# Kernel tuning notes

Measured on AMD Instinct MI355X. Metric: run time of the kernel, lower is better.

The kernel has to match this reference:

```python
import jax, jax.numpy as jnp
import numpy as np

N_NODES = 100000
N_EDGES = 1600000
H = 64
EPS_SM = 1e-16
NEG_SLOPE = 0.01  # LeakyReLU default
BN_EPS = 1e-5


def leaky_relu(x):
    return jnp.where(x >= 0, x, NEG_SLOPE * x)


def transformer_conv(x, src, tgt, edge_attr, Wq, bq, Wk, bk, Wv, bv, We, Ws, bs):
    # PyG TransformerConv, heads=1, concat=True, root_weight=True, lin_edge bias=False
    n = x.shape[0]
    q = x @ Wq + bq            # [N,H]
    k = x @ Wk + bk            # [N,H]
    v = x @ Wv + bv            # [N,H]
    e = edge_attr @ We         # [E,H]
    ke = k[src] + e            # [E,H]
    score = jnp.sum(q[tgt] * ke, axis=-1) / jnp.sqrt(jnp.float32(H))  # [E]
    # segment softmax over incoming edges of each target node
    m = jax.ops.segment_max(score, tgt, num_segments=n)
    m = jnp.where(jnp.isfinite(m), m, 0.0)
    p = jnp.exp(score - m[tgt])
    denom = jax.ops.segment_sum(p, tgt, num_segments=n)
    alpha = p / (denom[tgt] + EPS_SM)
    msg = (v[src] + e) * alpha[:, None]                  # [E,H]
    out = jax.ops.segment_sum(msg, tgt, num_segments=n)  # [N,H]
    return out + x @ Ws + bs


def batch_norm(x, gamma, beta):
    mean = jnp.mean(x, axis=0)
    var = jnp.mean((x - mean) ** 2, axis=0)
    return (x - mean) / jnp.sqrt(var + BN_EPS) * gamma + beta


def setup_inputs() -> dict:
    key = jax.random.key(0)
    ks = jax.random.split(key, 24)
    s = 0.05
    d = {
        "x": jax.random.normal(ks[0], (N_NODES, 2), jnp.float32),
        "edge_index": jax.random.randint(ks[1], (2, N_EDGES), 0, N_NODES, jnp.int32),
        "edge_attr": jax.random.normal(ks[2], (N_EDGES, 2), jnp.float32),
        "mask": jax.random.uniform(ks[3], (N_NODES,), jnp.float32),
        # gcn1 (in=2)
        "Wq1": jax.random.normal(ks[4], (2, H)) * s, "bq1": jnp.zeros((H,)),
        "Wk1": jax.random.normal(ks[5], (2, H)) * s, "bk1": jnp.zeros((H,)),
        "Wv1": jax.random.normal(ks[6], (2, H)) * s, "bv1": jnp.zeros((H,)),
        "We1": jax.random.normal(ks[7], (2, H)) * s,
        "Ws1": jax.random.normal(ks[8], (2, H)) * s, "bs1": jnp.zeros((H,)),
        # gcn2 (in=64)
        "Wq2": jax.random.normal(ks[9], (H, H)) * s, "bq2": jnp.zeros((H,)),
        "Wk2": jax.random.normal(ks[10], (H, H)) * s, "bk2": jnp.zeros((H,)),
        "Wv2": jax.random.normal(ks[11], (H, H)) * s, "bv2": jnp.zeros((H,)),
        "We2": jax.random.normal(ks[12], (2, H)) * s,
        "Ws2": jax.random.normal(ks[13], (H, H)) * s, "bs2": jnp.zeros((H,)),
        # batch norm
        "bn_gamma": jnp.ones((H,)), "bn_beta": jnp.zeros((H,)),
        # final MLP 64->32->1
        "Wf1": jax.random.normal(ks[14], (H, 32)) * s, "bf1": jnp.zeros((32,)),
        "Wf2": jax.random.normal(ks[15], (32, 1)) * s, "bf2": jnp.zeros((1,)),
        "iterations": 3,
    }
    return d


def reference(x, edge_index, edge_attr, mask,
              Wq1, bq1, Wk1, bk1, Wv1, bv1, We1, Ws1, bs1,
              Wq2, bq2, Wk2, bk2, Wv2, bv2, We2, Ws2, bs2,
              bn_gamma, bn_beta, Wf1, bf1, Wf2, bf2, iterations):
    src, tgt = edge_index[0], edge_index[1]
    h = transformer_conv(x, src, tgt, edge_attr, Wq1, bq1, Wk1, bk1, Wv1, bv1, We1, Ws1, bs1)
    h = leaky_relu(batch_norm(h, bn_gamma, bn_beta))
    h = leaky_relu(transformer_conv(h, src, tgt, edge_attr, Wq2, bq2, Wk2, bk2, Wv2, bv2, We2, Ws2, bs2))
    for _ in range(iterations - 1):
        h = leaky_relu(transformer_conv(h, src, tgt, edge_attr, Wq2, bq2, Wk2, bk2, Wv2, bv2, We2, Ws2, bs2))
    out = jnp.squeeze(leaky_relu(h @ Wf1 + bf1) @ Wf2 + bf2, axis=-1)  # [N]
    return out * mask
```

## Files before the change

### kernel.cpp

```cpp
#include <hip/hip_runtime.h>
#include <hip/hip_fp16.h>

#define N_NODES 100000
#define N_EDGES 1600000
#define SCAN_B ((N_NODES + 1023) / 1024)
#define BSHIFT 7
#define NB_BKT ((N_NODES + 127) / 128)
#define BCAP 2560

typedef _Float16 half2_t __attribute__((ext_vector_type(2)));
typedef _Float16 half8_t __attribute__((ext_vector_type(8)));
typedef float f32x4 __attribute__((ext_vector_type(4)));

__device__ __forceinline__ float lrelu(float x) { return x >= 0.f ? x : 0.01f * x; }

__global__ void k_count(const int* __restrict__ tgt, int* __restrict__ deg) {
    int i = blockIdx.x * 256 + threadIdx.x;
    atomicAdd(&deg[tgt[i]], 1);
}

__global__ void k_scan1(const int* __restrict__ deg, int* __restrict__ bsum) {
    __shared__ int s[256];
    int t = threadIdx.x;
    int gi = blockIdx.x * 1024 + t * 4;
// ... 202 lines not shown
    }
    bcomb[t] = v;
}

__global__ void k_prepw(const float* __restrict__ Wcomb, __half* __restrict__ wp) {
    int t = blockIdx.x * 256 + threadIdx.x;
    if (t >= 9216) return;
    int e = t & 7;
    int lane = (t >> 3) & 63;
    int kh = (t >> 9) & 1;
    int fm = t >> 10;
    int k = (kh << 5) + ((lane >> 4) << 3) + e;
    int c = fm * 16 + (lane & 15);
    wp[t] = __float2half(Wcomb[k * 144 + c]);
}

__global__ void k_prepv(const float* __restrict__ Wv, __half* __restrict__ wvp) {
    int t = blockIdx.x * 256 + threadIdx.x;
    if (t >= 4096) return;
    int e = t & 7;
    int lane = (t >> 3) & 63;
    int kh = (t >> 9) & 1;
    int fm = t >> 10;
    int k = (kh << 5) + ((lane >> 4) << 3) + e;
    int c = fm * 16 + (lane & 15);
    wvp[t] = __float2half(Wv[k * 64 + c]);
}

__global__ __launch_bounds__(256) void k_agg1(
    const float* __restrict__ x, const int* __restrict__ idx,
    const int2* __restrict__ csr, const float* __restrict__ Wv,
    const float* __restrict__ We, const float* __restrict__ Ws,
    const float* __restrict__ bv, const float* __restrict__ bs,
    const float* __restrict__ prep, float* __restrict__ o, int bucket) {
    int node = blockIdx.x * 4 + (threadIdx.x >> 6);
    int lane = threadIdx.x & 63;
    float2 xt = *(const float2*)&x[(size_t)node << 1];
    float a0 = xt.x * prep[0] + xt.y * prep[2] + prep[6];
    float a1 = xt.x * prep[1] + xt.y * prep[3] + prep[7];
    float b1 = xt.x * prep[4] + xt.y * prep[5] + prep[8];
    float g0 = xt.x * prep[9] + xt.y * prep[11] + prep[13];
    float g1 = xt.x * prep[10] + xt.y * prep[12] + prep[14];

    float l = 0.f, px0 = 0.f, px1 = 0.f, pA = 0.f, pB = 0.f;
    if (bucket) {
        int deg = idx[node];
        bool valid = lane < deg;
        int2 rec = valid ? csr[((size_t)node << 6) + lane] : make_int2(0, 0);
        int src = rec.x & 0xFFFFF;
        float2 ef = __half22float2(*(__half2*)&rec.y);
        float2 xs = valid ? *(const float2*)&x[(size_t)src << 1] : make_float2(0.f, 0.f);
        float t = a0 * xs.x + a1 * xs.y + b1 + g0 * ef.x + g1 * ef.y;
        float pp = valid ? __expf(t) : 0.f;
        l = pp;
        px0 = pp * xs.x;
        px1 = pp * xs.y;
        pA = pp * ef.x;
        pB = pp * ef.y;
    } else {
        int beg = idx[node], end = idx[node + 1];
        for (int p = beg + lane; p < end; p += 64) {
            int2 rec = csr[p];
            float2 ef = __half22float2(*(__half2*)&rec.y);
            float2 xs = *(const float2*)&x[(size_t)rec.x << 1];
            float t = a0 * xs.x + a1 * xs.y + b1 + g0 * ef.x + g1 * ef.y;
            float pp = __expf(t);
            l += pp;
            px0 += pp * xs.x;
            px1 += pp * xs.y;
            pA += pp * ef.x;
            pB += pp * ef.y;
        }
    }
#pragma unroll
    for (int D = 1; D < 64; D <<= 1) {
        l += __shfl_xor(l, D, 64);
        px0 += __shfl_xor(px0, D, 64);
        px1 += __shfl_xor(px1, D, 64);
        pA += __shfl_xor(pA, D, 64);
        pB += __shfl_xor(pB, D, 64);
    }
    float inv = 1.f / (l + 1e-16f);
    int c = lane;
    float r = (px0 * Wv[c] + px1 * Wv[64 + c] + pA * We[c] + pB * We[64 + c] +
               l * bv[c]) * inv +
              xt.x * Ws[c] + xt.y * Ws[64 + c] + bs[c];
    o[((size_t)node << 6) + c] = r;
}

__global__ void k_bnp(const float* __restrict__ o, float* __restrict__ bnsum,
                      float* __restrict__ bnsq) {
    __shared__ float s1[256], s2[256];
    int t = threadIdx.x;
    int c = t & 63, nsub = t >> 6;
    float su = 0.f, sq = 0.f;
    int base = blockIdx.x * 400;
    for (int i = 0; i < 100; i++) {
        int node = base + i * 4 + nsub;
        float v = o[((size_t)node << 6) + c];
        su += v;
        sq += v * v;
    }
    s1[t] = su;
    s2[t] = sq;
    __syncthreads();
    if (t < 64) {
        float a = s1[t] + s1[t + 64] + s1[t + 128] + s1[t + 192];
        float b = s2[t] + s2[t + 64] + s2[t + 128] + s2[t + 192];
        atomicAdd(&bnsum[t], a);
        atomicAdd(&bnsq[t], b);
    }
}

__global__ void k_bnf(const float* bnsum, const float* bnsq, const float* gamma,
                      const float* beta, float* bnab) {
    int c = threadIdx.x;
    float mean = bnsum[c] * (1.f / N_NODES);
    float var = bnsq[c] * (1.f / N_NODES) - mean * mean;
    float A = gamma[c] * rsqrtf(var + 1e-5f);
    bnab[c] = A;
    bnab[64 + c] = beta[c] - mean * A;
}

__global__ void k_bna(const float* __restrict__ o, const float* __restrict__ bnab,
                      float* __restrict__ h, __half* __restrict__ hh) {
    int idx = blockIdx.x * 256 + threadIdx.x;
    int c = idx & 63;
    float v = lrelu(o[idx] * bnab[c] + bnab[64 + c]);
    h[idx] = v;
    hh[idx] = __float2half(v);
}

__device__ __forceinline__ half8_t pack8(float4 lo, float4 hi) {
    half8_t r;
    r[0] = (_Float16)lo.x; r[1] = (_Float16)lo.y;
    r[2] = (_Float16)lo.z; r[3] = (_Float16)lo.w;
    r[4] = (_Float16)hi.x; r[5] = (_Float16)hi.y;
    r[6] = (_Float16)hi.z; r[7] = (_Float16)hi.w;
    return r;
}

__global__ __launch_bounds__(256) void k_gemm(
    const float* __restrict__ h, const __half* __restrict__ hhin,
    const __half* __restrict__ wp, const float* __restrict__ bcomb,
    const float* __restrict__ bnab, int use_bn,
    __half* __restrict__ qh, float* __restrict__ ext, __half* __restrict__ hhout) {
    __shared__ __half qsm[64 * 68];
    int tid = threadIdx.x;
    int w = tid >> 6;
    int lane = tid & 63;
    int nloc = lane & 15;
    int kg = lane >> 4;
    int base = blockIdx.x * 64;

    half8_t A[2], AE[2];
    const half8_t* wpv = (const half8_t*)wp;
#pragma unroll
    for (int kh = 0; kh < 2; kh++) A[kh] = wpv[((w << 1) + kh) * 64 + lane];
    if (w == 3) {
#pragma unroll
        for (int kh = 0; kh < 2; kh++) AE[kh] = wpv[((8 << 1) + kh) * 64 + lane];
    }

    half8_t z8;
#pragma unroll
    for (int i = 0; i < 8; i++) z8[i] = (_Float16)0.f;

    half8_t B[4][2];
    int n[4];
    bool g[4];
#pragma unroll
    for (int nf = 0; nf < 4; nf++) {
        n[nf] = base + (nf << 4) + nloc;
        g[nf] = n[nf] < N_NODES;
    }

    if (use_bn) {
        float4 bnA[2][2], bnB[2][2];
#pragma unroll
        for (int kh = 0; kh < 2; kh++) {
            int k0 = (kh << 5) + (kg << 3);
            bnA[kh][0] = *(const float4*)&bnab[k0];
            bnA[kh][1] = *(const float4*)&bnab[k0 + 4];
            bnB[kh][0] = *(const float4*)&bnab[64 + k0];
            bnB[kh][1] = *(const float4*)&bnab[64 + k0 + 4];
        }
        const float4 z4 = make_float4(0.f, 0.f, 0.f, 0.f);
#pragma unroll
        for (int nf = 0; nf < 4; nf++) {
            const float* hrow = h + ((size_t)n[nf] << 6);
#pragma unroll
            for (int kh = 0; kh < 2; kh++) {
                int k0 = (kh << 5) + (kg << 3);
                float4 lo = g[nf] ? *(const float4*)&hrow[k0] : z4;
                float4 hi = g[nf] ? *(const float4*)&hrow[k0 + 4] : z4;
                lo.x = lrelu(lo.x * bnA[kh][0].x + bnB[kh][0].x);
                lo.y = lrelu(lo.y * bnA[kh][0].y + bnB[kh][0].y);
                lo.z = lrelu(lo.z * bnA[kh][0].z + bnB[kh][0].z);
                lo.w = lrelu(lo.w * bnA[kh][0].w + bnB[kh][0].w);
                hi.x = lrelu(hi.x * bnA[kh][1].x + bnB[kh][1].x);
                hi.y = lrelu(hi.y * bnA[kh][1].y + bnB[kh][1].y);
                hi.z = lrelu(hi.z * bnA[kh][1].z + bnB[kh][1].z);
                hi.w = lrelu(hi.w * bnA[kh][1].w + bnB[kh][1].w);
                B[nf][kh] = pack8(lo, hi);
                if (g[nf]) *(half8_t*)&hhout[((size_t)n[nf] << 6) + k0] = B[nf][kh];
            }
        }
    } else {
#pragma unroll
        for (int nf = 0; nf < 4; nf++) {
#pragma unroll
            for (int kh = 0; kh < 2; kh++) {
                int k0 = (kh << 5) + (kg << 3);
                B[nf][kh] = g[nf] ? *(const half8_t*)&hhin[((size_t)n[nf] << 6) + k0]
                                  : z8;
            }
        }
    }

    f32x4 acc[4], accE[4];
#pragma unroll
    for (int nf = 0; nf < 4; nf++) {
        acc[nf] = (f32x4){0.f, 0.f, 0.f, 0.f};
        accE[nf] = (f32x4){0.f, 0.f, 0.f, 0.f};
    }

#pragma unroll
    for (int nf = 0; nf < 4; nf++) {
        acc[nf] = __builtin_amdgcn_mfma_f32_16x16x32_f16(A[0], B[nf][0], acc[nf],
                                                          0, 0, 0);
        acc[nf] = __builtin_amdgcn_mfma_f32_16x16x32_f16(A[1], B[nf][1], acc[nf],
                                                          0, 0, 0);
    }
    if (w == 3) {
#pragma unroll
        for (int nf = 0; nf < 4; nf++) {
            accE[nf] = __builtin_amdgcn_mfma_f32_16x16x32_f16(AE[0], B[nf][0],
                                                              accE[nf], 0, 0, 0);
// ... 9 lines not shown
    for (int nf = 0; nf < 4; nf++) {
        int nl = (nf << 4) + nloc;
        __half2 p0 = __floats2half2_rn(acc[nf][0] + bi.x, acc[nf][1] + bi.y);
        __half2 p1 = __floats2half2_rn(acc[nf][2] + bi.z, acc[nf][3] + bi.w);
        *(__half2*)&qsm[nl * 68 + c0] = p0;
        *(__half2*)&qsm[nl * 68 + c0 + 2] = p1;
    }
    if (w == 3 && kg == 0) {
        float4 be = *(const float4*)&bcomb[128];
#pragma unroll
        for (int nf = 0; nf < 4; nf++) {
            if (!g[nf]) continue;
            float4 r;
            r.x = accE[nf][0] + be.x;
            r.y = accE[nf][1] + be.y;
            r.z = accE[nf][2] + be.z;
            r.w = accE[nf][3] + be.w;
            *(float4*)&ext[(size_t)n[nf] << 2] = r;
        }
    }
    __syncthreads();
#pragma unroll
    for (int rep = 0; rep < 8; rep++) {
        int i = rep * 256 + tid;
        int row = i >> 5;
        int col = (i & 31) << 1;
        if (base + row < N_NODES) {
            int v = *(int*)&qsm[row * 68 + col];
            *(int*)&qh[((size_t)(base + row) << 6) + col] = v;
        }
    }
}

__global__ __launch_bounds__(256) void k_aggH(
    const __half* __restrict__ qh, const float* __restrict__ ext,
    const __half* __restrict__ hh, const int* __restrict__ idx,
    const int2* __restrict__ csr, __half* __restrict__ Shat,
    float* __restrict__ svec, int bucket) {
    __shared__ float red[4 * 64 * 20];
    int tid = threadIdx.x;
    int wv = tid >> 6;
    int node = blockIdx.x * 4 + wv;
    int lane = tid & 63;
    int es = lane >> 2;
    int cl = lane & 3;

    float4 ex = *(const float4*)&ext[(size_t)node << 2];
    float beta = ex.x, qe0 = ex.y, qe1 = ex.z;
    int4 qr0 = *(const int4*)&qh[((size_t)node << 6) + (cl << 4)];
    int4 qr1 = *(const int4*)&qh[((size_t)node << 6) + (cl << 4) + 8];
    const half2_t* qp0 = (const half2_t*)&qr0;
    const half2_t* qp1 = (const half2_t*)&qr1;

    float l = 0.f, sA = 0.f, sB = 0.f;
    float accv[16];
#pragma unroll
    for (int c = 0; c < 16; c++) accv[c] = 0.f;

    int nEdge, rbase;
    if (bucket) {
        nEdge = idx[node];
        rbase = node << 6;
    } else {
        rbase = idx[node];
        nEdge = idx[node + 1] - rbase;
    }
    int nIter = (nEdge + 15) >> 4;

    auto body = [&](int4 h0, int4 h1, int2 rec, bool ok) {
        const half2_t* hp0 = (const half2_t*)&h0;
        const half2_t* hp1 = (const half2_t*)&h1;
        float t = 0.f;
#if __has_builtin(__builtin_amdgcn_fdot2)
#pragma unroll
        for (int p = 0; p < 4; p++)
            t = __builtin_amdgcn_fdot2(hp0[p], qp0[p], t, false);
#pragma unroll
        for (int p = 0; p < 4; p++)
            t = __builtin_amdgcn_fdot2(hp1[p], qp1[p], t, false);
#else
        const __half* hq0 = (const __half*)&qr0;
        const __half* hq1 = (const __half*)&qr1;
        const __half* hh0 = (const __half*)&h0;
        const __half* hh1 = (const __half*)&h1;
#pragma unroll
        for (int c = 0; c < 8; c++) t += __half2float(hh0[c]) * __half2float(hq0[c]);
#pragma unroll
        for (int c = 0; c < 8; c++) t += __half2float(hh1[c]) * __half2float(hq1[c]);
#endif
        t += __shfl_xor(t, 1, 64);
        t += __shfl_xor(t, 2, 64);
        float2 ef = __half22float2(*(__half2*)&rec.y);
        t += beta + ef.x * qe0 + ef.y * qe1;
        float pp = ok ? __expf(t) : 0.f;
        l += pp;
        sA += pp * ef.x;
        sB += pp * ef.y;
        const __half* hs0 = (const __half*)&h0;
        const __half* hs1 = (const __half*)&h1;
#pragma unroll
        for (int c = 0; c < 8; c++) accv[c] += pp * __half2float(hs0[c]);
#pragma unroll
        for (int c = 0; c < 8; c++) accv[8 + c] += pp * __half2float(hs1[c]);
    };

    if (bucket) {
        int2 recs[4];
#pragma unroll
        for (int i = 0; i < 4; i++) {
            int e = (i << 4) + es;
            recs[i] = (e < nEdge) ? csr[(size_t)rbase + e] : make_int2(0, 0);
        }
        if (nIter > 0) {
            int src0 = recs[0].x & 0xFFFFF;
            const __half* hr = hh + ((size_t)src0 << 6) + (cl << 4);
            int4 h0c = *(const int4*)&hr[0];
            int4 h1c = *(const int4*)&hr[8];
#pragma unroll
            for (int i = 0; i < 4; i++) {
                if (i < nIter) {
                    int4 h0 = h0c, h1 = h1c;
                    if (i + 1 < nIter) {
                        int srcn = recs[i + 1].x & 0xFFFFF;
                        const __half* hrn = hh + ((size_t)srcn << 6) + (cl << 4);
                        h0c = *(const int4*)&hrn[0];
                        h1c = *(const int4*)&hrn[8];
                    }
                    body(h0, h1, recs[i], ((i << 4) + es) < nEdge);
                }
            }
        }
    } else {
        for (int i = 0; i < nIter; i++) {
            int e = (i << 4) + es;
            bool ok = e < nEdge;
            int2 rec = ok ? csr[(size_t)rbase + e] : make_int2(0, 0);
            int src = rec.x & 0xFFFFF;
            const __half* hr = hh + ((size_t)src << 6) + (cl << 4);
            int4 h0 = *(const int4*)&hr[0];
            int4 h1 = *(const int4*)&hr[8];
            body(h0, h1, rec, ok);
        }
    }

#pragma unroll
    for (int D = 4; D < 64; D <<= 1) {
        l += __shfl_xor(l, D, 64);
        sA += __shfl_xor(sA, D, 64);
        sB += __shfl_xor(sB, D, 64);
    }
    float inv = 1.f / (l + 1e-16f);

    float* my = &red[(wv * 64 + lane) * 20];
#pragma unroll
    for (int c = 0; c < 16; c += 4)
        *(float4*)&my[c] = make_float4(accv[c], accv[c + 1], accv[c + 2], accv[c + 3]);
    __asm__ volatile("" ::: "memory");
    float s = 0.f;
    int rb = wv * 64 * 20 + (lane >> 4) * 20 + (lane & 15);
#pragma unroll
    for (int es2 = 0; es2 < 16; es2++) s += red[rb + es2 * 80];
    Shat[((size_t)node << 6) + lane] = __float2half(s * inv);
    if (lane == 0)
        *(float4*)&svec[(size_t)node << 2] =
            make_float4(sA * inv, sB * inv, l * inv, 0.f);
}

__global__ __launch_bounds__(256) void k_proj(
    const __half* __restrict__ Shat, const float* __restrict__ svec,
    const __half* __restrict__ hh, const __half* __restrict__ wp,
    const __half* __restrict__ wvp, const float* __restrict__ We,
    const float* __restrict__ bv, const float* __restrict__ bcomb,
    float* __restrict__ hout, __half* __restrict__ hhout, int whh, int whout) {
    __shared__ float lds4[64 * 68];
    __half* hsm = (__half*)lds4;
    int tid = threadIdx.x;
    int w = tid >> 6;
    int lane = tid & 63;
    int nloc = lane & 15;
    int kg = lane >> 4;
    int base = blockIdx.x * 64;

    const half8_t* wv = (const half8_t*)wvp;
    const half8_t* wpv = (const half8_t*)wp;
    half8_t Av0 = wv[((w << 1) + 0) * 64 + lane];
    half8_t Av1 = wv[((w << 1) + 1) * 64 + lane];
    half8_t As0 = wpv[(((4 + w) << 1) + 0) * 64 + lane];
    half8_t As1 = wpv[(((4 + w) << 1) + 1) * 64 + lane];

    int rowg = kg << 2;
    int c0 = (w << 4) + rowg;
    float4 we0 = *(const float4*)&We[c0];
    float4 we1 = *(const float4*)&We[64 + c0];
    float4 bv4 = *(const float4*)&bv[c0];
    float4 bs4 = *(const float4*)&bcomb[64 + c0];

    half8_t z8;
#pragma unroll
    for (int i = 0; i < 8; i++) z8[i] = (_Float16)0.f;

#pragma unroll
    for (int nf = 0; nf < 4; nf++) {
        int n = base + (nf << 4) + nloc;
        bool g = n < N_NODES;
        const __half* srow = Shat + ((size_t)n << 6);
        const __half* hrow = hh + ((size_t)n << 6);
        half8_t Bs0 = g ? *(const half8_t*)&srow[(kg << 3)] : z8;
        half8_t Bs1 = g ? *(const half8_t*)&srow[32 + (kg << 3)] : z8;
        half8_t Bh0 = g ? *(const half8_t*)&hrow[(kg << 3)] : z8;
        half8_t Bh1 = g ? *(const half8_t*)&hrow[32 + (kg << 3)] : z8;

        f32x4 acc = (f32x4){0.f, 0.f, 0.f, 0.f};
        acc = __builtin_amdgcn_mfma_f32_16x16x32_f16(Av0, Bs0, acc, 0, 0, 0);
        acc = __builtin_amdgcn_mfma_f32_16x16x32_f16(Av1, Bs1, acc, 0, 0, 0);
        acc = __builtin_amdgcn_mfma_f32_16x16x32_f16(As0, Bh0, acc, 0, 0, 0);
        acc = __builtin_amdgcn_mfma_f32_16x16x32_f16(As1, Bh1, acc, 0, 0, 0);

        float4 sv = g ? *(const float4*)&svec[(size_t)n << 2]
                      : make_float4(0.f, 0.f, 0.f, 0.f);
        float4 r;
        r.x = lrelu(acc[0] + sv.x * we0.x + sv.y * we1.x + sv.z * bv4.x + bs4.x);
        r.y = lrelu(acc[1] + sv.x * we0.y + sv.y * we1.y + sv.z * bv4.y + bs4.y);
        r.z = lrelu(acc[2] + sv.x * we0.z + sv.y * we1.z + sv.z * bv4.z + bs4.z);
        r.w = lrelu(acc[3] + sv.x * we0.w + sv.y * we1.w + sv.z * bv4.w + bs4.w);

        int nl = (nf << 4) + nloc;
        if (whout) {
            *(float4*)&lds4[nl * 68 + c0] = r;
        } else {
            __half2 p0 = __floats2half2_rn(r.x, r.y);
            __half2 p1 = __floats2half2_rn(r.z, r.w);
            *(__half2*)&hsm[nl * 68 + c0] = p0;
            *(__half2*)&hsm[nl * 68 + c0 + 2] = p1;
        }
    }
    __syncthreads();
    if (whout) {
#pragma unroll
        for (int rep = 0; rep < 4; rep++) {
            int i = rep * 256 + tid;
            int row = i >> 4;
            int c4 = (i & 15) << 2;
            if (base + row < N_NODES) {
                float4 v = *(float4*)&lds4[row * 68 + c4];
                *(float4*)&hout[((size_t)(base + row) << 6) + c4] = v;
            }
        }
    } else {
#pragma unroll
        for (int rep = 0; rep < 8; rep++) {
            int i = rep * 256 + tid;
            int row = i >> 5;
            int col = (i & 31) << 1;
            if (base + row < N_NODES) {
                int v = *(int*)&hsm[row * 68 + col];
                *(int*)&hhout[((size_t)(base + row) << 6) + col] = v;
            }
        }
    }
}

__global__ __launch_bounds__(256) void k_mlp(const float* __restrict__ h,
                                             const float* __restrict__ Wf1,
                                             const float* __restrict__ bf1,
                                             const float* __restrict__ Wf2,
                                             const float* __restrict__ bf2v,
                                             const float* __restrict__ mask,
                                             float* __restrict__ out) {
    __shared__ float W1[64 * 32];
    __shared__ float W2[32];
    __shared__ float hsm[8][64];
    __shared__ float zs[256];
    int tid = threadIdx.x;
    for (int i = tid; i < 2048; i += 256) W1[i] = Wf1[i];
    if (tid < 32) W2[tid] = Wf2[tid];
    int base = blockIdx.x * 8;
    for (int i = tid; i < 512; i += 256) {
        int n = i >> 6, c = i & 63;
        hsm[n][c] = h[(base + n) * 64 + c];
    }
    __syncthreads();
    int n = tid >> 5, j = tid & 31;
    float acc = bf1[j];
    for (int c = 0; c < 64; c++) acc += hsm[n][c] * W1[c * 32 + j];
    zs[tid] = lrelu(acc) * W2[j];
    __syncthreads();
    if (j == 0) {
        int node = base + n;
        float r = bf2v[0];
        for (int jj = 0; jj < 32; jj++) r += zs[(n << 5) + jj];
        out[node] = r * mask[node];
    }
}

extern "C" void kernel_launch(void* const* d_in, const int* in_sizes, int n_in,
                              void* d_out, int out_size, void* d_ws, size_t ws_size,
                              hipStream_t stream) {
    const float* x = (const float*)d_in[0];
    const int* ei = (const int*)d_in[1];
    const float* ea = (const float*)d_in[2];
    const float* mask = (const float*)d_in[3];
    const float *Wq1 = (const float*)d_in[4], *bq1 = (const float*)d_in[5];
    const float *Wk1 = (const float*)d_in[6], *bk1 = (const float*)d_in[7];
    const float *Wv1 = (const float*)d_in[8], *bv1 = (const float*)d_in[9];
    const float *We1 = (const float*)d_in[10];
    const float *Ws1 = (const float*)d_in[11], *bs1 = (const float*)d_in[12];
    const float *Wq2 = (const float*)d_in[13], *bq2 = (const float*)d_in[14];
    const float *Wk2 = (const float*)d_in[15], *bk2 = (const float*)d_in[16];
    const float *Wv2 = (const float*)d_in[17], *bv2 = (const float*)d_in[18];
    const float *We2 = (const float*)d_in[19];
    const float *Ws2 = (const float*)d_in[20], *bs2 = (const float*)d_in[21];
    const float *gamma = (const float*)d_in[22], *beta = (const float*)d_in[23];
    const float *Wf1 = (const float*)d_in[24], *bf1 = (const float*)d_in[25];
    const float *Wf2 = (const float*)d_in[26], *bf2v = (const float*)d_in[27];
    float* out = (float*)d_out;

    const size_t bucket_need =
        (size_t)NB_BKT * BCAP * 8 + (size_t)N_NODES * 64 * 8 +
        (size_t)N_NODES * 64 * 4 * 2 + (size_t)N_NODES * 64 * 2 * 4 +
        (size_t)N_NODES * 16 * 2 + (size_t)N_NODES * 4 * 3 + (1 << 20);
    bool use_bucket = ws_size >= bucket_need;

    char* ws = (char*)d_ws;
    size_t off = 0;
    auto alloc = [&](size_t b) {
        size_t r = off;
        off += (b + 255) & ~(size_t)255;
        return r;
    };
    int* deg = (int*)(ws + alloc(N_NODES * 4));
    int* fill = (int*)(ws + alloc(N_NODES * 4));
    int* rowptr = (int*)(ws + alloc((N_NODES + 1) * 4));
    int* bsum = (int*)(ws + alloc(SCAN_B * 4));
    int* gCur = (int*)(ws + alloc(NB_BKT * 4));
    float* bnsum = (float*)(ws + alloc(64 * 4));
    float* bnsq = (float*)(ws + alloc(64 * 4));
    float* bnab = (float*)(ws + alloc(128 * 4));
    float* Wcomb = (float*)(ws + alloc(9216 * 4));
    float* bcomb = (float*)(ws + alloc(160 * 4));
    __half* wp = (__half*)(ws + alloc(9216 * 2));
    __half* wvp = (__half*)(ws + alloc(4096 * 2));
    float* ext = (float*)(ws + alloc((size_t)N_NODES * 16));
    float* svec = (float*)(ws + alloc((size_t)N_NODES * 16));
    int2* bin1 = (int2*)(ws + alloc(use_bucket ? (size_t)NB_BKT * BCAP * 8 : 256));
    int2* csr = (int2*)(ws + alloc(use_bucket ? (size_t)N_NODES * 64 * 8
                                              : (size_t)N_EDGES * 8));
    __half* qh = (__half*)(ws + alloc((size_t)N_NODES * 64 * 2));
    __half* Shat = (__half*)(ws + alloc((size_t)N_NODES * 64 * 2));
    __half* hh0 = (__half*)(ws + alloc((size_t)N_NODES * 64 * 2));
    __half* hh1 = (__half*)(ws + alloc((size_t)N_NODES * 64 * 2));
    float* hbuf = (float*)(ws + alloc((size_t)N_NODES * 64 * 4));
    float* obuf = (float*)(ws + alloc((size_t)N_NODES * 64 * 4));

    const int* srcI = ei;
    const int* tgtI = ei + N_EDGES;

    hipMemsetAsync(bnsum, 0, 64 * 4, stream);
    hipMemsetAsync(bnsq, 0, 64 * 4, stream);

    k_prep2<<<36, 256, 0, stream>>>(Wq2, Wk2, Ws2, We2, bk2, Wcomb);
    k_prepb<<<1, 192, 0, stream>>>(Wk2, We2, bq2, bk2, bs2, Wq1, Wk1, We1, bq1, bk1,
                                   bcomb);
    k_prepw<<<36, 256, 0, stream>>>(Wcomb, wp);
    k_prepv<<<16, 256, 0, stream>>>(Wv2, wvp);

    const int* aggIdx;
    if (use_bucket) {
        hipMemsetAsync(gCur, 0, NB_BKT * 4, stream);
        k_bin1<<<250, 256, 0, stream>>>(srcI, tgtI, (const float2*)ea, gCur, bin1);
        k_bin2<<<NB_BKT, 256, 0, stream>>>(gCur, bin1, csr, fill);
        aggIdx = fill;
    } else {
        hipMemsetAsync(deg, 0, N_NODES * 4, stream);
        k_count<<<N_EDGES / 256, 256, 0, stream>>>(tgtI, deg);
        k_scan1<<<SCAN_B, 256, 0, stream>>>(deg, bsum);
        k_scan2<<<1, 64, 0, stream>>>(bsum, rowptr);
        k_scan3<<<SCAN_B, 256, 0, stream>>>(deg, bsum, rowptr, fill);
        k_scatter<<<N_EDGES / 256, 256, 0, stream>>>(srcI, tgtI, (const float2*)ea,
                                                     fill, csr);
        aggIdx = rowptr;
    }
    int bkt = use_bucket ? 1 : 0;

    k_agg1<<<N_NODES / 4, 256, 0, stream>>>(x, aggIdx, csr, Wv1, We1, Ws1, bv1, bs1,
                                            bcomb + 144, obuf, bkt);
    k_bnp<<<250, 256, 0, stream>>>(obuf, bnsum, bnsq);
    k_bnf<<<1, 64, 0, stream>>>(bnsum, bnsq, gamma, beta, bnab);
    if (!use_bucket)
        k_bna<<<N_NODES * 64 / 256, 256, 0, stream>>>(obuf, bnab, hbuf, hh0);

    const int gemm_grid = (N_NODES + 63) / 64;
    for (int it = 0; it < 3; ++it) {
        int bnflag = (it == 0 && use_bucket) ? 1 : 0;
        const __half* hhG = (it == 1) ? hh1 : hh0;
        __half* hhP = (it == 0) ? hh1 : hh0;
        k_gemm<<<gemm_grid, 256, 0, stream>>>(obuf, hhG, wp, bcomb, bnab, bnflag,
                                              qh, ext, (__half*)hhG);
        k_aggH<<<N_NODES / 4, 256, 0, stream>>>(qh, ext, hhG, aggIdx, csr, Shat,
                                                svec, bkt);
        k_proj<<<gemm_grid, 256, 0, stream>>>(Shat, svec, hhG, wp, wvp, We2, bv2,
                                              bcomb, hbuf, hhP, (it < 2) ? 1 : 0,
                                              (it == 2) ? 1 : 0);
    }
    k_mlp<<<N_NODES / 8, 256, 0, stream>>>(hbuf, Wf1, bf1, Wf2, bf2v, mask, out);
}
```

Measured before the change: 571.5 us.

## Fuse aggregation, projection, next-layer GEMM and final MLP into one kernel

```diff
diff --git a/kernel.cpp b/kernel.cpp
--- a/kernel.cpp
+++ b/kernel.cpp
@@ -258,7 +258,7 @@
     const int2* __restrict__ csr, const float* __restrict__ Wv,
     const float* __restrict__ We, const float* __restrict__ Ws,
     const float* __restrict__ bv, const float* __restrict__ bs,
-    const float* __restrict__ prep, float* __restrict__ o, int bucket) {
+    const float* __restrict__ prep, __half* __restrict__ oh, int bucket) {
     int node = blockIdx.x * 4 + (threadIdx.x >> 6);
     int lane = threadIdx.x & 63;
     float2 xt = *(const float2*)&x[(size_t)node << 1];
@@ -311,10 +311,10 @@
     float r = (px0 * Wv[c] + px1 * Wv[64 + c] + pA * We[c] + pB * We[64 + c] +
                l * bv[c]) * inv +
               xt.x * Ws[c] + xt.y * Ws[64 + c] + bs[c];
-    o[((size_t)node << 6) + c] = r;
-}
-
-__global__ void k_bnp(const float* __restrict__ o, float* __restrict__ bnsum,
+    oh[((size_t)node << 6) + c] = __float2half(r);
+}
+
+__global__ void k_bnp(const __half* __restrict__ oh, float* __restrict__ bnsum,
                       float* __restrict__ bnsq) {
     __shared__ float s1[256], s2[256];
     int t = threadIdx.x;
@@ -323,7 +323,7 @@
     int base = blockIdx.x * 400;
     for (int i = 0; i < 100; i++) {
         int node = base + i * 4 + nsub;
-        float v = o[((size_t)node << 6) + c];
+        float v = __half2float(oh[((size_t)node << 6) + c]);
         su += v;
         sq += v * v;
     }
@@ -348,26 +348,16 @@
     bnab[64 + c] = beta[c] - mean * A;
 }
 
-__global__ void k_bna(const float* __restrict__ o, const float* __restrict__ bnab,
-                      float* __restrict__ h, __half* __restrict__ hh) {
+__global__ void k_bna(const __half* __restrict__ oh, const float* __restrict__ bnab,
+                      __half* __restrict__ hh) {
     int idx = blockIdx.x * 256 + threadIdx.x;
     int c = idx & 63;
-    float v = lrelu(o[idx] * bnab[c] + bnab[64 + c]);
-    h[idx] = v;
+    float v = lrelu(__half2float(oh[idx]) * bnab[c] + bnab[64 + c]);
     hh[idx] = __float2half(v);
 }
 
-__device__ __forceinline__ half8_t pack8(float4 lo, float4 hi) {
-    half8_t r;
-    r[0] = (_Float16)lo.x; r[1] = (_Float16)lo.y;
-    r[2] = (_Float16)lo.z; r[3] = (_Float16)lo.w;
-    r[4] = (_Float16)hi.x; r[5] = (_Float16)hi.y;
-    r[6] = (_Float16)hi.z; r[7] = (_Float16)hi.w;
-    return r;
-}
-
 __global__ __launch_bounds__(256) void k_gemm(
-    const float* __restrict__ h, const __half* __restrict__ hhin,
+    const __half* __restrict__ oh, const __half* __restrict__ hhin,
     const __half* __restrict__ wp, const float* __restrict__ bcomb,
     const float* __restrict__ bnab, int use_bn,
     __half* __restrict__ qh, float* __restrict__ ext, __half* __restrict__ hhout) {
@@ -411,25 +401,35 @@
             bnB[kh][0] = *(const float4*)&bnab[64 + k0];
             bnB[kh][1] = *(const float4*)&bnab[64 + k0 + 4];
         }
-        const float4 z4 = make_float4(0.f, 0.f, 0.f, 0.f);
+        const int4 zi4 = make_int4(0, 0, 0, 0);
 #pragma unroll
         for (int nf = 0; nf < 4; nf++) {
-            const float* hrow = h + ((size_t)n[nf] << 6);
+            const __half* orow = oh + ((size_t)n[nf] << 6);
 #pragma unroll
             for (int kh = 0; kh < 2; kh++) {
                 int k0 = (kh << 5) + (kg << 3);
-                float4 lo = g[nf] ? *(const float4*)&hrow[k0] : z4;
-                float4 hi = g[nf] ? *(const float4*)&hrow[k0 + 4] : z4;
-                lo.x = lrelu(lo.x * bnA[kh][0].x + bnB[kh][0].x);
-                lo.y = lrelu(lo.y * bnA[kh][0].y + bnB[kh][0].y);
-                lo.z = lrelu(lo.z * bnA[kh][0].z + bnB[kh][0].z);
-                lo.w = lrelu(lo.w * bnA[kh][0].w + bnB[kh][0].w);
-                hi.x = lrelu(hi.x * bnA[kh][1].x + bnB[kh][1].x);
-                hi.y = lrelu(hi.y * bnA[kh][1].y + bnB[kh][1].y);
-                hi.z = lrelu(hi.z * bnA[kh][1].z + bnB[kh][1].z);
-                hi.w = lrelu(hi.w * bnA[kh][1].w + bnB[kh][1].w);
-                B[nf][kh] = pack8(lo, hi);
-                if (g[nf]) *(half8_t*)&hhout[((size_t)n[nf] << 6) + k0] = B[nf][kh];
+                int4 raw = g[nf] ? *(const int4*)&orow[k0] : zi4;
+                const __half2* op = (const __half2*)&raw;
+                float2 o01 = __half22float2(op[0]);
+                float2 o23 = __half22float2(op[1]);
+                float2 o45 = __half22float2(op[2]);
+                float2 o67 = __half22float2(op[3]);
+                float4 lo, hi;
+                lo.x = lrelu(o01.x * bnA[kh][0].x + bnB[kh][0].x);
+                lo.y = lrelu(o01.y * bnA[kh][0].y + bnB[kh][0].y);
+                lo.z = lrelu(o23.x * bnA[kh][0].z + bnB[kh][0].z);
+                lo.w = lrelu(o23.y * bnA[kh][0].w + bnB[kh][0].w);
+                hi.x = lrelu(o45.x * bnA[kh][1].x + bnB[kh][1].x);
+                hi.y = lrelu(o45.y * bnA[kh][1].y + bnB[kh][1].y);
+                hi.z = lrelu(o67.x * bnA[kh][1].z + bnB[kh][1].z);
+                hi.w = lrelu(o67.y * bnA[kh][1].w + bnB[kh][1].w);
+                half8_t r;
+                r[0] = (_Float16)lo.x; r[1] = (_Float16)lo.y;
+                r[2] = (_Float16)lo.z; r[3] = (_Float16)lo.w;
+                r[4] = (_Float16)hi.x; r[5] = (_Float16)hi.y;
+                r[6] = (_Float16)hi.z; r[7] = (_Float16)hi.w;
+                B[nf][kh] = r;
+                if (g[nf]) *(half8_t*)&hhout[((size_t)n[nf] << 6) + k0] = r;
             }
         }
     } else {
@@ -505,264 +505,306 @@
     }
 }
 
-__global__ __launch_bounds__(256) void k_aggH(
-    const __half* __restrict__ qh, const float* __restrict__ ext,
-    const __half* __restrict__ hh, const int* __restrict__ idx,
-    const int2* __restrict__ csr, __half* __restrict__ Shat,
-    float* __restrict__ svec, int bucket) {
-    __shared__ float red[4 * 64 * 20];
+__global__ __launch_bounds__(256) void k_fused(
+    __half* qh, float* ext,
+    const __half* __restrict__ hh_in, __half* __restrict__ hh_out,
+    const int* __restrict__ idx, const int2* __restrict__ csr,
+    const __half* __restrict__ wp, const __half* __restrict__ wvp,
+    const float* __restrict__ We, const float* __restrict__ bv,
+    const float* __restrict__ bcomb,
+    const float* __restrict__ Wf1, const float* __restrict__ bf1,
+    const float* __restrict__ Wf2, const float* __restrict__ bf2v,
+    const float* __restrict__ mask, float* __restrict__ out,
+    int last, int bucket) {
+    __shared__ __align__(16) char smem[20480 + 9216 + 1024];
+    float* red = (float*)smem;
+    __half* rsm16 = (__half*)smem;
+    float* rsm32 = (float*)smem;
+    __half* Shatsm = (__half*)(smem + 20480);
+    __half* qsm = (__half*)(smem + 20480);
+    float* W1sm = (float*)(smem + 20480);
+    float4* svecsm = (float4*)(smem + 20480 + 9216);
+
     int tid = threadIdx.x;
     int wv = tid >> 6;
-    int node = blockIdx.x * 4 + wv;
     int lane = tid & 63;
-    int es = lane >> 2;
-    int cl = lane & 3;
-
-    float4 ex = *(const float4*)&ext[(size_t)node << 2];
-    float beta = ex.x, qe0 = ex.y, qe1 = ex.z;
-    int4 qr0 = *(const int4*)&qh[((size_t)node << 6) + (cl << 4)];
-    int4 qr1 = *(const int4*)&qh[((size_t)node << 6) + (cl << 4) + 8];
-    const half2_t* qp0 = (const half2_t*)&qr0;
-    const half2_t* qp1 = (const half2_t*)&qr1;
-
-    float l = 0.f, sA = 0.f, sB = 0.f;
-    float accv[16];
-#pragma unroll
-    for (int c = 0; c < 16; c++) accv[c] = 0.f;
-
-    int nEdge, rbase;
-    if (bucket) {
-        nEdge = idx[node];
-        rbase = node << 6;
-    } else {
-        rbase = idx[node];
-        nEdge = idx[node + 1] - rbase;
-    }
-    int nIter = (nEdge + 15) >> 4;
-
-    auto body = [&](int4 h0, int4 h1, int2 rec, bool ok) {
-        const half2_t* hp0 = (const half2_t*)&h0;
-        const half2_t* hp1 = (const half2_t*)&h1;
-        float t = 0.f;
+    int base = blockIdx.x * 64;
+
+    {
+        int es = lane >> 2, cl = lane & 3;
+        float* myred = &red[(wv * 64 + lane) * 20];
+        int rb = wv * 64 * 20 + (lane >> 4) * 20 + (lane & 15);
+        for (int nl = 0; nl < 16; nl++) {
+            int node = base + (wv << 4) + nl;
+            if (node >= N_NODES) continue;
+            float4 ex = *(const float4*)&ext[(size_t)node << 2];
+            float beta = ex.x, qe0 = ex.y, qe1 = ex.z;
+            int4 qr0 = *(const int4*)&qh[((size_t)node << 6) + (cl << 4)];
+            int4 qr1 = *(const int4*)&qh[((size_t)node << 6) + (cl << 4) + 8];
+            const half2_t* qp0 = (const half2_t*)&qr0;
+            const half2_t* qp1 = (const half2_t*)&qr1;
+
+            float l = 0.f, sA = 0.f, sB = 0.f;
+            float accv[16];
+#pragma unroll
+            for (int c = 0; c < 16; c++) accv[c] = 0.f;
+
+            int nEdge, rbase2;
+            if (bucket) {
+                nEdge = idx[node];
+                rbase2 = node << 6;
+            } else {
+                rbase2 = idx[node];
+                nEdge = idx[node + 1] - rbase2;
+            }
+            int nIter = (nEdge + 15) >> 4;
+
+            auto body = [&](int4 h0, int4 h1, int2 rec, bool ok) {
+                const half2_t* hp0 = (const half2_t*)&h0;
+                const half2_t* hp1 = (const half2_t*)&h1;
+                float t = 0.f;
 #if __has_builtin(__builtin_amdgcn_fdot2)
 #pragma unroll
-        for (int p = 0; p < 4; p++)
-            t = __builtin_amdgcn_fdot2(hp0[p], qp0[p], t, false);
-#pragma unroll
-        for (int p = 0; p < 4; p++)
-            t = __builtin_amdgcn_fdot2(hp1[p], qp1[p], t, false);
+                for (int p = 0; p < 4; p++)
+                    t = __builtin_amdgcn_fdot2(hp0[p], qp0[p], t, false);
+#pragma unroll
+                for (int p = 0; p < 4; p++)
+                    t = __builtin_amdgcn_fdot2(hp1[p], qp1[p], t, false);
 #else
-        const __half* hq0 = (const __half*)&qr0;
-        const __half* hq1 = (const __half*)&qr1;
-        const __half* hh0 = (const __half*)&h0;
-        const __half* hh1 = (const __half*)&h1;
-#pragma unroll
-        for (int c = 0; c < 8; c++) t += __half2float(hh0[c]) * __half2float(hq0[c]);
-#pragma unroll
-        for (int c = 0; c < 8; c++) t += __half2float(hh1[c]) * __half2float(hq1[c]);
+                const __half* hq0 = (const __half*)&qr0;
+                const __half* hq1 = (const __half*)&qr1;
+                const __half* hh0 = (const __half*)&h0;
+                const __half* hh1 = (const __half*)&h1;
+#pragma unroll
+                for (int c = 0; c < 8; c++)
+                    t += __half2float(hh0[c]) * __half2float(hq0[c]);
+#pragma unroll
+                for (int c = 0; c < 8; c++)
+                    t += __half2float(hh1[c]) * __half2float(hq1[c]);
 #endif
-        t += __shfl_xor(t, 1, 64);
-        t += __shfl_xor(t, 2, 64);
-        float2 ef = __half22float2(*(__half2*)&rec.y);
-        t += beta + ef.x * qe0 + ef.y * qe1;
-        float pp = ok ? __expf(t) : 0.f;
-        l += pp;
-        sA += pp * ef.x;
-        sB += pp * ef.y;
-        const __half* hs0 = (const __half*)&h0;
-        const __half* hs1 = (const __half*)&h1;
-#pragma unroll
-        for (int c = 0; c < 8; c++) accv[c] += pp * __half2float(hs0[c]);
-#pragma unroll
-        for (int c = 0; c < 8; c++) accv[8 + c] += pp * __half2float(hs1[c]);
-    };
-
-    if (bucket) {
-        int2 recs[4];
-#pragma unroll
-        for (int i = 0; i < 4; i++) {
-            int e = (i << 4) + es;
-            recs[i] = (e < nEdge) ? csr[(size_t)rbase + e] : make_int2(0, 0);
-        }
-        if (nIter > 0) {
-            int src0 = recs[0].x & 0xFFFFF;
-            const __half* hr = hh + ((size_t)src0 << 6) + (cl << 4);
-            int4 h0c = *(const int4*)&hr[0];
-            int4 h1c = *(const int4*)&hr[8];
-#pragma unroll
-            for (int i = 0; i < 4; i++) {
-                if (i < nIter) {
-                    int4 h0 = h0c, h1 = h1c;
-                    if (i + 1 < nIter) {
-                        int srcn = recs[i + 1].x & 0xFFFFF;
-                        const __half* hrn = hh + ((size_t)srcn << 6) + (cl << 4);
-                        h0c = *(const int4*)&hrn[0];
-                        h1c = *(const int4*)&hrn[8];
+                t += __shfl_xor(t, 1, 64);
+                t += __shfl_xor(t, 2, 64);
+                float2 ef = __half22float2(*(__half2*)&rec.y);
+                t += beta + ef.x * qe0 + ef.y * qe1;
+                float pp = ok ? __expf(t) : 0.f;
+                l += pp;
+                sA += pp * ef.x;
+                sB += pp * ef.y;
+                const __half* hs0 = (const __half*)&h0;
+                const __half* hs1 = (const __half*)&h1;
+#pragma unroll
+                for (int c = 0; c < 8; c++) accv[c] += pp * __half2float(hs0[c]);
+#pragma unroll
+                for (int c = 0; c < 8; c++) accv[8 + c] += pp * __half2float(hs1[c]);
+            };
+
+            if (bucket) {
+                int2 recs[4];
+#pragma unroll
+                for (int i = 0; i < 4; i++) {
+                    int e = (i << 4) + es;
+                    recs[i] = (e < nEdge) ? csr[(size_t)rbase2 + e] : make_int2(0, 0);
+                }
+                if (nIter > 0) {
+                    int src0 = recs[0].x & 0xFFFFF;
+                    const __half* hr = hh_in + ((size_t)src0 << 6) + (cl << 4);
+                    int4 h0c = *(const int4*)&hr[0];
+                    int4 h1c = *(const int4*)&hr[8];
+#pragma unroll
+                    for (int i = 0; i < 4; i++) {
+                        if (i < nIter) {
+                            int4 h0 = h0c, h1 = h1c;
+                            if (i + 1 < nIter) {
+                                int srcn = recs[i + 1].x & 0xFFFFF;
+                                const __half* hrn =
+                                    hh_in + ((size_t)srcn << 6) + (cl << 4);
+                                h0c = *(const int4*)&hrn[0];
+                                h1c = *(const int4*)&hrn[8];
+                            }
+                            body(h0, h1, recs[i], ((i << 4) + es) < nEdge);
+                        }
                     }
-                    body(h0, h1, recs[i], ((i << 4) + es) < nEdge);
+                }
+            } else {
+                for (int i = 0; i < nIter; i++) {
+                    int e = (i << 4) + es;
+                    bool ok = e < nEdge;
+                    int2 rec = ok ? csr[(size_t)rbase2 + e] : make_int2(0, 0);
+                    int src = rec.x & 0xFFFFF;
+                    const __half* hr = hh_in + ((size_t)src << 6) + (cl << 4);
+                    int4 h0 = *(const int4*)&hr[0];
+                    int4 h1 = *(const int4*)&hr[8];
+                    body(h0, h1, rec, ok);
                 }
             }
-        }
-    } else {
-        for (int i = 0; i < nIter; i++) {
-            int e = (i << 4) + es;
-            bool ok = e < nEdge;
-            int2 rec = ok ? csr[(size_t)rbase + e] : make_int2(0, 0);
-            int src = rec.x & 0xFFFFF;
-            const __half* hr = hh + ((size_t)src << 6) + (cl << 4);
-            int4 h0 = *(const int4*)&hr[0];
-            int4 h1 = *(const int4*)&hr[8];
-            body(h0, h1, rec, ok);
-        }
-    }
-
-#pragma unroll
-    for (int D = 4; D < 64; D <<= 1) {
-        l += __shfl_xor(l, D, 64);
-        sA += __shfl_xor(sA, D, 64);
-        sB += __shfl_xor(sB, D, 64);
-    }
-    float inv = 1.f / (l + 1e-16f);
-
-    float* my = &red[(wv * 64 + lane) * 20];
-#pragma unroll
-    for (int c = 0; c < 16; c += 4)
-        *(float4*)&my[c] = make_float4(accv[c], accv[c + 1], accv[c + 2], accv[c + 3]);
-    __asm__ volatile("" ::: "memory");
-    float s = 0.f;
-    int rb = wv * 64 * 20 + (lane >> 4) * 20 + (lane & 15);
-#pragma unroll
-    for (int es2 = 0; es2 < 16; es2++) s += red[rb + es2 * 80];
-    Shat[((size_t)node << 6) + lane] = __float2half(s * inv);
-    if (lane == 0)
-        *(float4*)&svec[(size_t)node << 2] =
-            make_float4(sA * inv, sB * inv, l * inv, 0.f);
-}
-
-__global__ __launch_bounds__(256) void k_proj(
-    const __half* __restrict__ Shat, const float* __restrict__ svec,
-    const __half* __restrict__ hh, const __half* __restrict__ wp,
-    const __half* __restrict__ wvp, const float* __restrict__ We,
-    const float* __restrict__ bv, const float* __restrict__ bcomb,
-    float* __restrict__ hout, __half* __restrict__ hhout, int whh, int whout) {
-    __shared__ float lds4[64 * 68];
-    __half* hsm = (__half*)lds4;
-    int tid = threadIdx.x;
-    int w = tid >> 6;
-    int lane = tid & 63;
-    int nloc = lane & 15;
-    int kg = lane >> 4;
-    int base = blockIdx.x * 64;
-
-    const half8_t* wv = (const half8_t*)wvp;
-    const half8_t* wpv = (const half8_t*)wp;
-    half8_t Av0 = wv[((w << 1) + 0) * 64 + lane];
-    half8_t Av1 = wv[((w << 1) + 1) * 64 + lane];
-    half8_t As0 = wpv[(((4 + w) << 1) + 0) * 64 + lane];
-    half8_t As1 = wpv[(((4 + w) << 1) + 1) * 64 + lane];
-
-    int rowg = kg << 2;
-    int c0 = (w << 4) + rowg;
-    float4 we0 = *(const float4*)&We[c0];
-    float4 we1 = *(const float4*)&We[64 + c0];
-    float4 bv4 = *(const float4*)&bv[c0];
-    float4 bs4 = *(const float4*)&bcomb[64 + c0];
-
-    half8_t z8;
-#pragma unroll
-    for (int i = 0; i < 8; i++) z8[i] = (_Float16)0.f;
-
-#pragma unroll
-    for (int nf = 0; nf < 4; nf++) {
-        int n = base + (nf << 4) + nloc;
-        bool g = n < N_NODES;
-        const __half* srow = Shat + ((size_t)n << 6);
-        const __half* hrow = hh + ((size_t)n << 6);
-        half8_t Bs0 = g ? *(const half8_t*)&srow[(kg << 3)] : z8;
-        half8_t Bs1 = g ? *(const half8_t*)&srow[32 + (kg << 3)] : z8;
-        half8_t Bh0 = g ? *(const half8_t*)&hrow[(kg << 3)] : z8;
-        half8_t Bh1 = g ? *(const half8_t*)&hrow[32 + (kg << 3)] : z8;
-
-        f32x4 acc = (f32x4){0.f, 0.f, 0.f, 0.f};
-        acc = __builtin_amdgcn_mfma_f32_16x16x32_f16(Av0, Bs0, acc, 0, 0, 0);
-        acc = __builtin_amdgcn_mfma_f32_16x16x32_f16(Av1, Bs1, acc, 0, 0, 0);
-        acc = __builtin_amdgcn_mfma_f32_16x16x32_f16(As0, Bh0, acc, 0, 0, 0);
-        acc = __builtin_amdgcn_mfma_f32_16x16x32_f16(As1, Bh1, acc, 0, 0, 0);
-
-        float4 sv = g ? *(const float4*)&svec[(size_t)n << 2]
-                      : make_float4(0.f, 0.f, 0.f, 0.f);
-        float4 r;
-        r.x = lrelu(acc[0] + sv.x * we0.x + sv.y * we1.x + sv.z * bv4.x + bs4.x);
-        r.y = lrelu(acc[1] + sv.x * we0.y + sv.y * we1.y + sv.z * bv4.y + bs4.y);
-        r.z = lrelu(acc[2] + sv.x * we0.z + sv.y * we1.z + sv.z * bv4.z + bs4.z);
-        r.w = lrelu(acc[3] + sv.x * we0.w + sv.y * we1.w + sv.z * bv4.w + bs4.w);
-
-        int nl = (nf << 4) + nloc;
-        if (whout) {
-            *(float4*)&lds4[nl * 68 + c0] = r;
-        } else {
-            __half2 p0 = __floats2half2_rn(r.x, r.y);
-            __half2 p1 = __floats2half2_rn(r.z, r.w);
-            *(__half2*)&hsm[nl * 68 + c0] = p0;
-            *(__half2*)&hsm[nl * 68 + c0 + 2] = p1;
-        }
-    }
-    __syncthreads();
-    if (whout) {
-#pragma unroll
-        for (int rep = 0; rep < 4; rep++) {
-            int i = rep * 256 + tid;
-            int row = i >> 4;
-            int c4 = (i & 15) << 2;
-            if (base + row < N_NODES) {
-                float4 v = *(float4*)&lds4[row * 68 + c4];
-                *(float4*)&hout[((size_t)(base + row) << 6) + c4] = v;
+
+#pragma unroll
+            for (int D = 4; D < 64; D <<= 1) {
+                l += __shfl_xor(l, D, 64);
+                sA += __shfl_xor(sA, D, 64);
+                sB += __shfl_xor(sB, D, 64);
             }
-        }
-    } else {
+            float inv = 1.f / (l + 1e-16f);
+
+#pragma unroll
+            for (int c = 0; c < 16; c += 4)
+                *(float4*)&myred[c] =
+                    make_float4(accv[c], accv[c + 1], accv[c + 2], accv[c + 3]);
+            __asm__ volatile("" ::: "memory");
+            float s = 0.f;
+#pragma unroll
+            for (int es2 = 0; es2 < 16; es2++) s += red[rb + es2 * 80];
+            Shatsm[((wv << 4) + nl) * 72 + lane] = __float2half(s * inv);
+            if (lane == 0)
+                svecsm[(wv << 4) + nl] = make_float4(sA * inv, sB * inv, l * inv, 0.f);
+            __asm__ volatile("" ::: "memory");
+        }
+    }
+    __syncthreads();
+
+    {
+        int nloc = lane & 15, kg = lane >> 4;
+        const half8_t* wvv = (const half8_t*)wvp;
+        const half8_t* wpv = (const half8_t*)wp;
+        half8_t Av0 = wvv[((wv << 1) + 0) * 64 + lane];
+        half8_t Av1 = wvv[((wv << 1) + 1) * 64 + lane];
+        half8_t As0 = wpv[(((4 + wv) << 1) + 0) * 64 + lane];
+        half8_t As1 = wpv[(((4 + wv) << 1) + 1) * 64 + lane];
+
+        int rowg = kg << 2;
+        int c0 = (wv << 4) + rowg;
+        float4 we0 = *(const float4*)&We[c0];
+        float4 we1 = *(const float4*)&We[64 + c0];
+        float4 bv4 = *(const float4*)&bv[c0];
+        float4 bs4 = *(const float4*)&bcomb[64 + c0];
+
+        half8_t z8;
+#pragma unroll
+        for (int i = 0; i < 8; i++) z8[i] = (_Float16)0.f;
+
+#pragma unroll
+        for (int nf = 0; nf < 4; nf++) {
+            int n = base + (nf << 4) + nloc;
+            bool g = n < N_NODES;
+            int nl2 = (nf << 4) + nloc;
+            const __half* srow = &Shatsm[nl2 * 72];
+            const __half* hrow = hh_in + ((size_t)n << 6);
+            half8_t Bs0 = g ? *(const half8_t*)&srow[kg << 3] : z8;
+            half8_t Bs1 = g ? *(const half8_t*)&srow[32 + (kg << 3)] : z8;
+            half8_t Bh0 = g ? *(const half8_t*)&hrow[kg << 3] : z8;
+            half8_t Bh1 = g ? *(const half8_t*)&hrow[32 + (kg << 3)] : z8;
+
+            f32x4 acc = (f32x4){0.f, 0.f, 0.f, 0.f};
+            acc = __builtin_amdgcn_mfma_f32_16x16x32_f16(Av0, Bs0, acc, 0, 0, 0);
+            acc = __builtin_amdgcn_mfma_f32_16x16x32_f16(Av1, Bs1, acc, 0, 0, 0);
+            acc = __builtin_amdgcn_mfma_f32_16x16x32_f16(As0, Bh0, acc, 0, 0, 0);
+            acc = __builtin_amdgcn_mfma_f32_16x16x32_f16(As1, Bh1, acc, 0, 0, 0);
+
+            float4 sv = g ? svecsm[nl2] : make_float4(0.f, 0.f, 0.f, 0.f);
+            float4 r;
+            r.x = lrelu(acc[0] + sv.x * we0.x + sv.y * we1.x + sv.z * bv4.x + bs4.x);
+            r.y = lrelu(acc[1] + sv.x * we0.y + sv.y * we1.y + sv.z * bv4.y + bs4.y);
+            r.z = lrelu(acc[2] + sv.x * we0.z + sv.y * we1.z + sv.z * bv4.z + bs4.z);
+            r.w = lrelu(acc[3] + sv.x * we0.w + sv.y * we1.w + sv.z * bv4.w + bs4.w);
+
+            if (last) {
+                *(float4*)&rsm32[nl2 * 68 + c0] = r;
+            } else {
+                __half2 p0 = __floats2half2_rn(r.x, r.y);
+                __half2 p1 = __floats2half2_rn(r.z, r.w);
+                *(__half2*)&rsm16[nl2 * 72 + c0] = p0;
+                *(__half2*)&rsm16[nl2 * 72 + c0 + 2] = p1;
+            }
+        }
+    }
+    __syncthreads();
+
+    if (!last) {
+        int nloc = lane & 15, kg = lane >> 4;
+        const half8_t* wpv = (const half8_t*)wp;
+        half8_t A0 = wpv[((wv << 1) + 0) * 64 + lane];
+        half8_t A1 = wpv[((wv << 1) + 1) * 64 + lane];
+        half8_t AE0 = A0, AE1 = A1;
+        if (wv == 3) {
+            AE0 = wpv[16 * 64 + lane];
+            AE1 = wpv[17 * 64 + lane];
+        }
+        int rowg = kg << 2;
+        int c0 = (wv << 4) + rowg;
+        float4 bi = *(const float4*)&bcomb[c0];
+
+#pragma unroll
+        for (int nf = 0; nf < 4; nf++) {
+            int nl2 = (nf << 4) + nloc;
+            const __half* rrow = &rsm16[nl2 * 72];
+            half8_t B0 = *(const half8_t*)&rrow[kg << 3];
+            half8_t B1 = *(const half8_t*)&rrow[32 + (kg << 3)];
+            f32x4 acc = (f32x4){0.f, 0.f, 0.f, 0.f};
+            acc = __builtin_amdgcn_mfma_f32_16x16x32_f16(A0, B0, acc, 0, 0, 0);
+            acc = __builtin_amdgcn_mfma_f32_16x16x32_f16(A1, B1, acc, 0, 0, 0);
+            __half2 p0 = __floats2half2_rn(acc[0] + bi.x, acc[1] + bi.y);
+            __half2 p1 = __floats2half2_rn(acc[2] + bi.z, acc[3] + bi.w);
+            *(__half2*)&qsm[nl2 * 72 + c0] = p0;
+            *(__half2*)&qsm[nl2 * 72 + c0 + 2] = p1;
+            if (wv == 3) {
+                f32x4 ae = (f32x4){0.f, 0.f, 0.f, 0.f};
+                ae = __builtin_amdgcn_mfma_f32_16x16x32_f16(AE0, B0, ae, 0, 0, 0);
+                ae = __builtin_amdgcn_mfma_f32_16x16x32_f16(AE1, B1, ae, 0, 0, 0);
+                if (kg == 0) {
+                    int n = base + nl2;
+                    if (n < N_NODES) {
+                        float4 be = *(const float4*)&bcomb[128];
+                        float4 r;
+                        r.x = ae[0] + be.x;
+                        r.y = ae[1] + be.y;
+                        r.z = ae[2] + be.z;
+                        r.w = ae[3] + be.w;
+                        *(float4*)&ext[(size_t)n << 2] = r;
+                    }
+                }
+            }
+        }
+        __syncthreads();
 #pragma unroll
         for (int rep = 0; rep < 8; rep++) {
             int i = rep * 256 + tid;
             int row = i >> 5;
             int col = (i & 31) << 1;
             if (base + row < N_NODES) {
-                int v = *(int*)&hsm[row * 68 + col];
-                *(int*)&hhout[((size_t)(base + row) << 6) + col] = v;
+                *(int*)&qh[((size_t)(base + row) << 6) + col] =
+                    *(int*)&qsm[row * 72 + col];
+                *(int*)&hh_out[((size_t)(base + row) << 6) + col] =
+                    *(int*)&rsm16[row * 72 + col];
             }
         }
-    }
-}
-
-__global__ __launch_bounds__(256) void k_mlp(const float* __restrict__ h,
-                                             const float* __restrict__ Wf1,
-                                             const float* __restrict__ bf1,
-                                             const float* __restrict__ Wf2,
-                                             const float* __restrict__ bf2v,
-                                             const float* __restrict__ mask,
-                                             float* __restrict__ out) {
-    __shared__ float W1[64 * 32];
-    __shared__ float W2[32];
-    __shared__ float hsm[8][64];
-    __shared__ float zs[256];
-    int tid = threadIdx.x;
-    for (int i = tid; i < 2048; i += 256) W1[i] = Wf1[i];
-    if (tid < 32) W2[tid] = Wf2[tid];
-    int base = blockIdx.x * 8;
-    for (int i = tid; i < 512; i += 256) {
-        int n = i >> 6, c = i & 63;
-        hsm[n][c] = h[(base + n) * 64 + c];
-    }
-    __syncthreads();
-    int n = tid >> 5, j = tid & 31;
-    float acc = bf1[j];
-    for (int c = 0; c < 64; c++) acc += hsm[n][c] * W1[c * 32 + j];
-    zs[tid] = lrelu(acc) * W2[j];
-    __syncthreads();
-    if (j == 0) {
-        int node = base + n;
-        float r = bf2v[0];
-        for (int jj = 0; jj < 32; jj++) r += zs[(n << 5) + jj];
-        out[node] = r * mask[node];
+    } else {
+        for (int i = tid; i < 2048; i += 256) W1sm[i] = Wf1[i];
+        __syncthreads();
+        int nl2 = tid >> 2, jg = tid & 3;
+        int node = base + nl2;
+        float a8[8];
+        const float* b1p = &bf1[jg << 3];
+#pragma unroll
+        for (int k = 0; k < 8; k++) a8[k] = b1p[k];
+        const float* hr = &rsm32[nl2 * 68];
+        for (int c = 0; c < 64; c++) {
+            float hv = hr[c];
+            const float* wr = &W1sm[(c << 5) + (jg << 3)];
+            float4 wa = *(const float4*)&wr[0];
+            float4 wb = *(const float4*)&wr[4];
+            a8[0] += hv * wa.x; a8[1] += hv * wa.y;
+            a8[2] += hv * wa.z; a8[3] += hv * wa.w;
+            a8[4] += hv * wb.x; a8[5] += hv * wb.y;
+            a8[6] += hv * wb.z; a8[7] += hv * wb.w;
+        }
+        const float* w2p = &Wf2[jg << 3];
+        float zs = 0.f;
+#pragma unroll
+        for (int k = 0; k < 8; k++) zs += lrelu(a8[k]) * w2p[k];
+        zs += __shfl_xor(zs, 1, 64);
+        zs += __shfl_xor(zs, 2, 64);
+        if (jg == 0 && node < N_NODES)
+            out[node] = (zs + bf2v[0]) * mask[node];
     }
 }
 
@@ -790,8 +832,9 @@
 
     const size_t bucket_need =
         (size_t)NB_BKT * BCAP * 8 + (size_t)N_NODES * 64 * 8 +
-        (size_t)N_NODES * 64 * 4 * 2 + (size_t)N_NODES * 64 * 2 * 4 +
-        (size_t)N_NODES * 16 * 2 + (size_t)N_NODES * 4 * 3 + (1 << 20);
+        (size_t)N_NODES * 64 * 2 * 4 +
+        (size_t)N_NODES * 16 +
+        (size_t)N_NODES * 4 * 3 + (1 << 20);
     bool use_bucket = ws_size >= bucket_need;
 
     char* ws = (char*)d_ws;
@@ -814,16 +857,13 @@
     __half* wp = (__half*)(ws + alloc(9216 * 2));
     __half* wvp = (__half*)(ws + alloc(4096 * 2));
     float* ext = (float*)(ws + alloc((size_t)N_NODES * 16));
-    float* svec = (float*)(ws + alloc((size_t)N_NODES * 16));
     int2* bin1 = (int2*)(ws + alloc(use_bucket ? (size_t)NB_BKT * BCAP * 8 : 256));
     int2* csr = (int2*)(ws + alloc(use_bucket ? (size_t)N_NODES * 64 * 8
                                               : (size_t)N_EDGES * 8));
     __half* qh = (__half*)(ws + alloc((size_t)N_NODES * 64 * 2));
-    __half* Shat = (__half*)(ws + alloc((size_t)N_NODES * 64 * 2));
+    __half* oh = (__half*)(ws + alloc((size_t)N_NODES * 64 * 2));
     __half* hh0 = (__half*)(ws + alloc((size_t)N_NODES * 64 * 2));
     __half* hh1 = (__half*)(ws + alloc((size_t)N_NODES * 64 * 2));
-    float* hbuf = (float*)(ws + alloc((size_t)N_NODES * 64 * 4));
-    float* obuf = (float*)(ws + alloc((size_t)N_NODES * 64 * 4));
 
     const int* srcI = ei;
     const int* tgtI = ei + N_EDGES;
@@ -856,24 +896,22 @@
     int bkt = use_bucket ? 1 : 0;
 
     k_agg1<<<N_NODES / 4, 256, 0, stream>>>(x, aggIdx, csr, Wv1, We1, Ws1, bv1, bs1,
-                                            bcomb + 144, obuf, bkt);
-    k_bnp<<<250, 256, 0, stream>>>(obuf, bnsum, bnsq);
+                                            bcomb + 144, oh, bkt);
+    k_bnp<<<250, 256, 0, stream>>>(oh, bnsum, bnsq);
     k_bnf<<<1, 64, 0, stream>>>(bnsum, bnsq, gamma, beta, bnab);
     if (!use_bucket)
-        k_bna<<<N_NODES * 64 / 256, 256, 0, stream>>>(obuf, bnab, hbuf, hh0);
+        k_bna<<<N_NODES * 64 / 256, 256, 0, stream>>>(oh, bnab, hh0);
 
     const int gemm_grid = (N_NODES + 63) / 64;
-    for (int it = 0; it < 3; ++it) {
-        int bnflag = (it == 0 && use_bucket) ? 1 : 0;
-        const __half* hhG = (it == 1) ? hh1 : hh0;
-        __half* hhP = (it == 0) ? hh1 : hh0;
-        k_gemm<<<gemm_grid, 256, 0, stream>>>(obuf, hhG, wp, bcomb, bnab, bnflag,
-                                              qh, ext, (__half*)hhG);
-        k_aggH<<<N_NODES / 4, 256, 0, stream>>>(qh, ext, hhG, aggIdx, csr, Shat,
-                                                svec, bkt);
-        k_proj<<<gemm_grid, 256, 0, stream>>>(Shat, svec, hhG, wp, wvp, We2, bv2,
-                                              bcomb, hbuf, hhP, (it < 2) ? 1 : 0,
-                                              (it == 2) ? 1 : 0);
-    }
-    k_mlp<<<N_NODES / 8, 256, 0, stream>>>(hbuf, Wf1, bf1, Wf2, bf2v, mask, out);
-}
+    k_gemm<<<gemm_grid, 256, 0, stream>>>(oh, hh0, wp, bcomb, bnab, bkt, qh, ext,
+                                          hh0);
+    k_fused<<<gemm_grid, 256, 0, stream>>>(qh, ext, hh0, hh1, aggIdx, csr, wp, wvp,
+                                           We2, bv2, bcomb, Wf1, bf1, Wf2, bf2v,
+                                           mask, out, 0, bkt);
+    k_fused<<<gemm_grid, 256, 0, stream>>>(qh, ext, hh1, hh0, aggIdx, csr, wp, wvp,
+                                           We2, bv2, bcomb, Wf1, bf1, Wf2, bf2v,
+                                           mask, out, 0, bkt);
+    k_fused<<<gemm_grid, 256, 0, stream>>>(qh, ext, hh0, hh1, aggIdx, csr, wp, wvp,
+                                           We2, bv2, bcomb, Wf1, bf1, Wf2, bf2v,
+                                           mask, out, 1, bkt);
+}
```

Result: faster. 533.5 us (-6.6%).
